# Performance work log

Measured on AMD Instinct MI355X. Metric: run time of the kernel, lower is better.

## Reference

```python
import jax, jax.numpy as jnp
import numpy as np

B, N = 64, 4096          # batch of diagrams, points per diagram
H, W = 64, 64            # persistence-image resolution
L, R = 5, 256            # num_landscapes, landscape resolution
EPS = 1e-8


def setup_inputs() -> dict:
    key = jax.random.key(0)
    k1, = jax.random.split(key, 1)
    u = jax.random.uniform(k1, (B, N, 2), dtype=jnp.float32)
    birth = u[..., 0] * 0.5                      # births in [0, 0.5]
    death = birth + u[..., 1] * 0.5 + 1e-3       # deaths > births, in range
    pairs = jnp.stack([birth, death], axis=-1)   # (B, N, 2)
    sigma = jnp.float32(0.1)                     # learned bandwidth (nn.Parameter)
    return {"pairs": pairs, "sigma": sigma}


def reference(pairs, sigma):
    # ---- Persistence image (batched, vectorized over points) ----
    grid_x = jnp.linspace(0.0, 1.0, W, dtype=pairs.dtype)   # birth axis
    grid_y = jnp.linspace(0.0, 1.0, H, dtype=pairs.dtype)   # persistence axis
    birth = pairs[..., 0]                 # (B, N)
    death = pairs[..., 1]                 # (B, N)
    pers = death - birth                  # (B, N)
    # normalization per config ranges (0,1): divide by (range + 1e-8)
    birth_n = birth / (1.0 + EPS)
    pers_n = pers / (1.0 + EPS)
    weights = pers                        # weight_fn == 'linear'
    inv2s2 = 1.0 / (2.0 * sigma * sigma)
    # separable Gaussian factors: (B, N, W) and (B, N, H)
    gx = jnp.exp(-(grid_x[None, None, :] - birth_n[..., None]) ** 2 * inv2s2)
    gy = jnp.exp(-(grid_y[None, None, :] - pers_n[..., None]) ** 2 * inv2s2)
    # sum_n wt_n * gy_n(h) * gx_n(w)  ->  (B, H, W)
    image = jnp.einsum('bnh,bnw->bhw', gy * weights[..., None], gx)
    image = image / (jnp.max(image, axis=(1, 2), keepdims=True) + EPS)

    # ---- Persistence landscapes ----
    min_b = jnp.min(birth, axis=1, keepdims=True)   # (B, 1)
    max_d = jnp.max(death, axis=1, keepdims=True)   # (B, 1)
    frac = jnp.linspace(0.0, 1.0, R, dtype=pairs.dtype)
    t = min_b + (max_d - min_b) * frac[None, :]     # (B, R)
    rising = jnp.clip(t[:, None, :] - birth[..., None], 0.0)   # (B, N, R)
    falling = jnp.clip(death[..., None] - t[:, None, :], 0.0)  # (B, N, R)
    tents = jnp.minimum(rising, falling)                        # (B, N, R)
    # descending sort over points + take top L == top_k over point axis
    top = jax.lax.top_k(jnp.swapaxes(tents, 1, 2), L)[0]        # (B, R, L)
    landscapes = jnp.swapaxes(top, 1, 2)                        # (B, L, R)
    return image, landscapes
```

## Files before the change

### kernel.cpp

```cpp
#include <hip/hip_runtime.h>
#include <math.h>


#define B_   64
#define N_   4096
#define HW_  64
#define RES_ 256
#define EPSF 1e-8f
#define KC_  4
#define CPB  1024
#define KP   64
#define LPB_ 8
#define LCH  128

typedef short short8v  __attribute__((ext_vector_type(8)));
typedef float float4v  __attribute__((ext_vector_type(4)));

__device__ __forceinline__ unsigned short f2bf(float f) {
    unsigned int u = __float_as_uint(f);
    u += 0x7fffu + ((u >> 16) & 1u);
    return (unsigned short)(u >> 16);
}

#define INS5(v0, v1, v2, v3, v4, x)                       \
    {                                                     \
        float _p0 = v0, _p1 = v1, _p2 = v2, _p3 = v3;     \
        v0 = fmaxf(_p0, x);                               \
        v1 = __builtin_amdgcn_fmed3f(_p0, _p1, x);        \
        v2 = __builtin_amdgcn_fmed3f(_p1, _p2, x);        \
        v3 = __builtin_amdgcn_fmed3f(_p2, _p3, x);        \
        v4 = __builtin_amdgcn_fmed3f(_p3, v4, x);         \
    }

union SmemU {
    struct {
        unsigned short gy[64 * 72];
        unsigned short gx[64 * 72];
        float2 pts[CPB];
    } img;
    struct {
        float lmerge[4 * 5 * RES_];
        float red[8];
    } land;
};

__global__ __launch_bounds__(256) void k_main(const float* __restrict__ pairs,
                                              const float* __restrict__ sigp,
                                              float* __restrict__ part,
                                              float* __restrict__ lp,
                                              int* __restrict__ ctr,
                                              float* __restrict__ out) {
    __shared__ SmemU sm;
    __shared__ int last_flag;
    __shared__ float redf[4];

    int tid = threadIdx.x;
    int l = tid & 63, w = tid >> 6;

    if (blockIdx.x < 256) {
        int kc = blockIdx.x & 3, b = blockIdx.x >> 2;
        float sigma = sigp[0];
        float cc = 0.5f / (sigma * sigma);

        const float4* src = (const float4*)(pairs + 2 * ((size_t)b * N_ + kc * CPB));
        ((float4*)sm.img.pts)[tid]       = src[tid];
        ((float4*)sm.img.pts)[256 + tid] = src[256 + tid];

        int c  = tid & 63;
        int pg = tid >> 6;
        float xc = (float)c * (1.0f / 63.0f);

        float4v acc[4];
        #pragma unroll
        for (int c4 = 0; c4 < 4; ++c4) acc[c4] = (float4v){0.f, 0.f, 0.f, 0.f};

        int rowA = (w * 16 + (l & 15)) * 72 + (l >> 4) * 8;

        for (int ch = 0; ch < CPB / KP; ++ch) {
            __syncthreads();
            int p0 = ch * KP + pg * 16;
            alignas(16) unsigned short gyb[16], gxb[16];
            #pragma unroll
            for (int j = 0; j < 16; ++j) {
                float2 q = sm.img.pts[p0 + j];
                float pe = q.y - q.x;
                float dx = xc - q.x;
                float dy = xc - pe;
                gxb[j] = f2bf(__expf(-dx * dx * cc));
                gyb[j] = f2bf(pe * __expf(-dy * dy * cc));
            }
            *(uint4*)&sm.img.gy[c * 72 + pg * 16]     = *(uint4*)&gyb[0];
            *(uint4*)&sm.img.gy[c * 72 + pg * 16 + 8] = *(uint4*)&gyb[8];
            *(uint4*)&sm.img.gx[c * 72 + pg * 16]     = *(uint4*)&gxb[0];
            *(uint4*)&sm.img.gx[c * 72 + pg * 16 + 8] = *(uint4*)&gxb[8];
            __syncthreads();
            #pragma unroll
            for (int ks = 0; ks < 2; ++ks) {
                short8v af = *(const short8v*)&sm.img.gy[rowA + ks * 32];
                #pragma unroll
                for (int c4 = 0; c4 < 4; ++c4) {
                    short8v bf = *(const short8v*)
                        &sm.img.gx[(c4 * 16 + (l & 15)) * 72 + ks * 32 + (l >> 4) * 8];
                    acc[c4] = __builtin_amdgcn_mfma_f32_16x16x32_bf16(af, bf, acc[c4], 0, 0, 0);
                }
            }
        }

        float* dst = part + (size_t)(b * KC_ + kc) * (HW_ * HW_);
        #pragma unroll
        for (int c4 = 0; c4 < 4; ++c4)
            #pragma unroll
            for (int reg = 0; reg < 4; ++reg) {
                int h = w * 16 + (l >> 4) * 4 + reg;
                int wv = c4 * 16 + (l & 15);
                dst[h * HW_ + wv] = acc[c4][reg];
            }

        __syncthreads();
        if (tid == 0) {
            int old = __hip_atomic_fetch_add(&ctr[b], 1, __ATOMIC_ACQ_REL,
                                             __HIP_MEMORY_SCOPE_AGENT);
            last_flag = (old == KC_ - 1);
        }
        __syncthreads();
        if (last_flag) {
            const float4* p0 = (const float4*)(part + (size_t)b * KC_ * (HW_ * HW_));
            float4 s[4];
            float m = 0.0f;
            #pragma unroll
            for (int i = 0; i < 4; ++i) {
                int pix4 = tid + i * 256;
                float4 v = p0[pix4];
                #pragma unroll
                for (int k2 = 1; k2 < KC_; ++k2) {
                    float4 u = p0[(size_t)k2 * 1024 + pix4];
                    v.x += u.x; v.y += u.y; v.z += u.z; v.w += u.w;
                }
                s[i] = v;
                m = fmaxf(m, fmaxf(fmaxf(v.x, v.y), fmaxf(v.z, v.w)));
            }
            #pragma unroll
            for (int off = 32; off > 0; off >>= 1) m = fmaxf(m, __shfl_xor(m, off, 64));
            if ((tid & 63) == 0) redf[tid >> 6] = m;
            __syncthreads();
            m = fmaxf(fmaxf(redf[0], redf[1]), fmaxf(redf[2], redf[3]));
            float inv = 1.0f / (m + EPSF);
            float4* od = (float4*)(out + (size_t)b * (HW_ * HW_));
            #pragma unroll
            for (int i = 0; i < 4; ++i) {
                float4 v = s[i];
                v.x *= inv; v.y *= inv; v.z *= inv; v.w *= inv;
                od[tid + i * 256] = v;
            }
        }
    } else {
        int idx = blockIdx.x - 256;
        int b = idx >> 3, pcb = idx & 7;

        const float4* pb4 = (const float4*)(pairs + 2 * (size_t)b * N_);
        float mn = 1e30f, mx = -1e30f;
        #pragma unroll
        for (int i = 0; i < 8; ++i) {
            float4 q = pb4[tid + i * 256];
            mn = fminf(mn, fminf(q.x, q.z));
            mx = fmaxf(mx, fmaxf(q.y, q.w));
        }
        #pragma unroll
        for (int off = 32; off > 0; off >>= 1) {
            mn = fminf(mn, __shfl_xor(mn, off, 64));
            mx = fmaxf(mx, __shfl_xor(mx, off, 64));
        }
        if ((tid & 63) == 0) { sm.land.red[w] = mn; sm.land.red[4 + w] = mx; }
        __syncthreads();
        float minb = fminf(fminf(sm.land.red[0], sm.land.red[1]),
                           fminf(sm.land.red[2], sm.land.red[3]));
        float maxd = fmaxf(fmaxf(sm.land.red[4], sm.land.red[5]),
                           fmaxf(sm.land.red[6], sm.land.red[7]));

        int pc = pcb * 4 + w;
        float scl = (maxd - minb) * (1.0f / 255.0f);
        float t0 = minb + scl * (float)l;
        float t1 = t0 + scl * 64.0f;
        float t2 = t0 + scl * 128.0f;
        float t3 = t0 + scl * 192.0f;

        float a0 = 0.f, a1 = 0.f, a2 = 0.f, a3 = 0.f, a4 = 0.f;
        float b0 = 0.f, b1 = 0.f, b2 = 0.f, b3 = 0.f, b4 = 0.f;
        float c0 = 0.f, c1 = 0.f, c2 = 0.f, c3 = 0.f, c4 = 0.f;
        float d0 = 0.f, d1 = 0.f, d2 = 0.f, d3 = 0.f, d4 = 0.f;

        const float4* pw = (const float4*)(pairs + 2 * ((size_t)b * N_ + pc * LCH));
        #pragma unroll 4
        for (int p = 0; p < LCH / 2; ++p) {
            float4 q = pw[p];
            {
                float bb = q.x, dd = q.y;
                float x;
                x = fminf(t0 - bb, dd - t0); INS5(a0, a1, a2, a3, a4, x);
                x = fminf(t1 - bb, dd - t1); INS5(b0, b1, b2, b3, b4, x);
                x = fminf(t2 - bb, dd - t2); INS5(c0, c1, c2, c3, c4, x);
                x = fminf(t3 - bb, dd - t3); INS5(d0, d1, d2, d3, d4, x);
            }
            {
                float bb = q.z, dd = q.w;
                float x;
                x = fminf(t0 - bb, dd - t0); INS5(a0, a1, a2, a3, a4, x);
                x = fminf(t1 - bb, dd - t1); INS5(b0, b1, b2, b3, b4, x);
                x = fminf(t2 - bb, dd - t2); INS5(c0, c1, c2, c3, c4, x);
                x = fminf(t3 - bb, dd - t3); INS5(d0, d1, d2, d3, d4, x);
            }
        }

        __syncthreads();
        float* lm = sm.land.lmerge;
        lm[(w * 5 + 0) * RES_ + l]       = a0; lm[(w * 5 + 1) * RES_ + l]       = a1;
        lm[(w * 5 + 2) * RES_ + l]       = a2; lm[(w * 5 + 3) * RES_ + l]       = a3;
        lm[(w * 5 + 4) * RES_ + l]       = a4;
        lm[(w * 5 + 0) * RES_ + l + 64]  = b0; lm[(w * 5 + 1) * RES_ + l + 64]  = b1;
        lm[(w * 5 + 2) * RES_ + l + 64]  = b2; lm[(w * 5 + 3) * RES_ + l + 64]  = b3;
        lm[(w * 5 + 4) * RES_ + l + 64]  = b4;
        lm[(w * 5 + 0) * RES_ + l + 128] = c0; lm[(w * 5 + 1) * RES_ + l + 128] = c1;
        lm[(w * 5 + 2) * RES_ + l + 128] = c2; lm[(w * 5 + 3) * RES_ + l + 128] = c3;
        lm[(w * 5 + 4) * RES_ + l + 128] = c4;
        lm[(w * 5 + 0) * RES_ + l + 192] = d0; lm[(w * 5 + 1) * RES_ + l + 192] = d1;
        lm[(w * 5 + 2) * RES_ + l + 192] = d2; lm[(w * 5 + 3) * RES_ + l + 192] = d3;
        lm[(w * 5 + 4) * RES_ + l + 192] = d4;
        __syncthreads();

        float v0 = lm[0 * RES_ + tid], v1 = lm[1 * RES_ + tid], v2 = lm[2 * RES_ + tid],
              v3 = lm[3 * RES_ + tid], v4 = lm[4 * RES_ + tid];
        #pragma unroll
        for (int wv = 1; wv < 4; ++wv)
            #pragma unroll
            for (int lvl = 0; lvl < 5; ++lvl) {
                float x = lm[(wv * 5 + lvl) * RES_ + tid];
                INS5(v0, v1, v2, v3, v4, x);
            }
        float* dl = lp + (size_t)(b * LPB_ + pcb) * 5 * RES_;
        dl[0 * RES_ + tid] = v0; dl[1 * RES_ + tid] = v1; dl[2 * RES_ + tid] = v2;
        dl[3 * RES_ + tid] = v3; dl[4 * RES_ + tid] = v4;

        __syncthreads();
        if (tid == 0) {
            int old = __hip_atomic_fetch_add(&ctr[64 + b], 1, __ATOMIC_ACQ_REL,
                                             __HIP_MEMORY_SCOPE_AGENT);
            last_flag = (old == LPB_ - 1);
        }
        __syncthreads();
        if (last_flag) {
            const float* lpb = lp + (size_t)b * LPB_ * 5 * RES_;
            float u0 = lpb[0 * RES_ + tid], u1 = lpb[1 * RES_ + tid],
                  u2 = lpb[2 * RES_ + tid], u3 = lpb[3 * RES_ + tid],
                  u4 = lpb[4 * RES_ + tid];
            for (int p2 = 1; p2 < LPB_; ++p2) {
                #pragma unroll
                for (int lvl = 0; lvl < 5; ++lvl) {
                    float x = lpb[(p2 * 5 + lvl) * RES_ + tid];
                    INS5(u0, u1, u2, u3, u4, x);
                }
            }
            float* o = out + (size_t)B_ * HW_ * HW_ + (size_t)b * (5 * RES_);
            o[tid]            = u0;
            o[RES_ + tid]     = u1;
            o[2 * RES_ + tid] = u2;
            o[3 * RES_ + tid] = u3;
            o[4 * RES_ + tid] = u4;
        }
    }
}

extern "C" void kernel_launch(void* const* d_in, const int* in_sizes, int n_in,
                              void* d_out, int out_size, void* d_ws, size_t ws_size,
                              hipStream_t stream) {
    const float* pairs = (const float*)d_in[0];
    const float* sig   = (const float*)d_in[1];
    float* out = (float*)d_out;
    float* wsf = (float*)d_ws;

    int*   ctr  = (int*)wsf;
    float* part = wsf + 128;
    float* lp   = part + (size_t)B_ * KC_ * HW_ * HW_;

    hipMemsetAsync(ctr, 0, 128 * sizeof(int), stream);
    k_main<<<768, 256, 0, stream>>>(pairs, sig, part, lp, ctr, out);
}
```

Baseline: 102.5 us.

## Split into partial and finish kernels, double block splits, interleave roles

```diff
diff --git a/kernel.cpp b/kernel.cpp
--- a/kernel.cpp
+++ b/kernel.cpp
@@ -7,19 +7,18 @@
 #define HW_  64
 #define RES_ 256
 #define EPSF 1e-8f
-#define KC_  4
-#define CPB  1024
+#define KC_  8
+#define CPB  512
 #define KP   64
-#define LPB_ 8
-#define LCH  128
+#define LPB_ 16
+#define LCH  64
 
 typedef short short8v  __attribute__((ext_vector_type(8)));
 typedef float float4v  __attribute__((ext_vector_type(4)));
 
-__device__ __forceinline__ unsigned short f2bf(float f) {
-    unsigned int u = __float_as_uint(f);
-    u += 0x7fffu + ((u >> 16) & 1u);
-    return (unsigned short)(u >> 16);
+__device__ __forceinline__ unsigned pk_bf(float a, float b) {
+    unsigned ua = __float_as_uint(a), ub = __float_as_uint(b);
+    return ((ua + 0x8000u) >> 16) | ((ub + 0x8000u) & 0xffff0000u);
 }
 
 #define INS5(v0, v1, v2, v3, v4, x)                       \
@@ -36,7 +35,6 @@
     struct {
         unsigned short gy[64 * 72];
         unsigned short gx[64 * 72];
-        float2 pts[CPB];
     } img;
     struct {
         float lmerge[4 * 5 * RES_];
@@ -44,27 +42,20 @@
     } land;
 };
 
-__global__ __launch_bounds__(256) void k_main(const float* __restrict__ pairs,
-                                              const float* __restrict__ sigp,
-                                              float* __restrict__ part,
-                                              float* __restrict__ lp,
-                                              int* __restrict__ ctr,
-                                              float* __restrict__ out) {
+__global__ __launch_bounds__(256) void k_partial(const float* __restrict__ pairs,
+                                                 const float* __restrict__ sigp,
+                                                 float* __restrict__ part,
+                                                 float* __restrict__ lp) {
     __shared__ SmemU sm;
-    __shared__ int last_flag;
-    __shared__ float redf[4];
-
     int tid = threadIdx.x;
     int l = tid & 63, w = tid >> 6;
-
-    if (blockIdx.x < 256) {
-        int kc = blockIdx.x & 3, b = blockIdx.x >> 2;
+    int role = blockIdx.x % 3;
+    int id   = blockIdx.x / 3;
+
+    if (role == 0) {
+        int kc = id & 7, b = id >> 3;
         float sigma = sigp[0];
-        float cc = 0.5f / (sigma * sigma);
-
-        const float4* src = (const float4*)(pairs + 2 * ((size_t)b * N_ + kc * CPB));
-        ((float4*)sm.img.pts)[tid]       = src[tid];
-        ((float4*)sm.img.pts)[256 + tid] = src[256 + tid];
+        float ncc2 = -(0.5f / (sigma * sigma)) * 1.4426950408889634f;
 
         int c  = tid & 63;
         int pg = tid >> 6;
@@ -75,24 +66,29 @@
         for (int c4 = 0; c4 < 4; ++c4) acc[c4] = (float4v){0.f, 0.f, 0.f, 0.f};
 
         int rowA = (w * 16 + (l & 15)) * 72 + (l >> 4) * 8;
+        const float4* pb4 = (const float4*)(pairs + 2 * ((size_t)b * N_ + kc * CPB));
 
         for (int ch = 0; ch < CPB / KP; ++ch) {
+            int p0 = ch * 32 + pg * 8;
+            unsigned gxp[8], gyp[8];
+            #pragma unroll
+            for (int jp = 0; jp < 8; ++jp) {
+                float4 q = pb4[p0 + jp];
+                float pe0 = q.y - q.x, pe1 = q.w - q.z;
+                float dx0 = xc - q.x, dx1 = xc - q.z;
+                float dy0 = xc - pe0, dy1 = xc - pe1;
+                float ex0 = __builtin_amdgcn_exp2f(dx0 * dx0 * ncc2);
+                float ex1 = __builtin_amdgcn_exp2f(dx1 * dx1 * ncc2);
+                float ey0 = pe0 * __builtin_amdgcn_exp2f(dy0 * dy0 * ncc2);
+                float ey1 = pe1 * __builtin_amdgcn_exp2f(dy1 * dy1 * ncc2);
+                gxp[jp] = pk_bf(ex0, ex1);
+                gyp[jp] = pk_bf(ey0, ey1);
+            }
             __syncthreads();
-            int p0 = ch * KP + pg * 16;
-            alignas(16) unsigned short gyb[16], gxb[16];
-            #pragma unroll
-            for (int j = 0; j < 16; ++j) {
-                float2 q = sm.img.pts[p0 + j];
-                float pe = q.y - q.x;
-                float dx = xc - q.x;
-                float dy = xc - pe;
-                gxb[j] = f2bf(__expf(-dx * dx * cc));
-                gyb[j] = f2bf(pe * __expf(-dy * dy * cc));
-            }
-            *(uint4*)&sm.img.gy[c * 72 + pg * 16]     = *(uint4*)&gyb[0];
-            *(uint4*)&sm.img.gy[c * 72 + pg * 16 + 8] = *(uint4*)&gyb[8];
-            *(uint4*)&sm.img.gx[c * 72 + pg * 16]     = *(uint4*)&gxb[0];
-            *(uint4*)&sm.img.gx[c * 72 + pg * 16 + 8] = *(uint4*)&gxb[8];
+            *(uint4*)&sm.img.gy[c * 72 + pg * 16]     = *(uint4*)&gyp[0];
+            *(uint4*)&sm.img.gy[c * 72 + pg * 16 + 8] = *(uint4*)&gyp[4];
+            *(uint4*)&sm.img.gx[c * 72 + pg * 16]     = *(uint4*)&gxp[0];
+            *(uint4*)&sm.img.gx[c * 72 + pg * 16 + 8] = *(uint4*)&gxp[4];
             __syncthreads();
             #pragma unroll
             for (int ks = 0; ks < 2; ++ks) {
@@ -115,47 +111,9 @@
                 int wv = c4 * 16 + (l & 15);
                 dst[h * HW_ + wv] = acc[c4][reg];
             }
-
-        __syncthreads();
-        if (tid == 0) {
-            int old = __hip_atomic_fetch_add(&ctr[b], 1, __ATOMIC_ACQ_REL,
-                                             __HIP_MEMORY_SCOPE_AGENT);
-            last_flag = (old == KC_ - 1);
-        }
-        __syncthreads();
-        if (last_flag) {
-            const float4* p0 = (const float4*)(part + (size_t)b * KC_ * (HW_ * HW_));
-            float4 s[4];
-            float m = 0.0f;
-            #pragma unroll
-            for (int i = 0; i < 4; ++i) {
-                int pix4 = tid + i * 256;
-                float4 v = p0[pix4];
-                #pragma unroll
-                for (int k2 = 1; k2 < KC_; ++k2) {
-                    float4 u = p0[(size_t)k2 * 1024 + pix4];
-                    v.x += u.x; v.y += u.y; v.z += u.z; v.w += u.w;
-                }
-                s[i] = v;
-                m = fmaxf(m, fmaxf(fmaxf(v.x, v.y), fmaxf(v.z, v.w)));
-            }
-            #pragma unroll
-            for (int off = 32; off > 0; off >>= 1) m = fmaxf(m, __shfl_xor(m, off, 64));
-            if ((tid & 63) == 0) redf[tid >> 6] = m;
-            __syncthreads();
-            m = fmaxf(fmaxf(redf[0], redf[1]), fmaxf(redf[2], redf[3]));
-            float inv = 1.0f / (m + EPSF);
-            float4* od = (float4*)(out + (size_t)b * (HW_ * HW_));
-            #pragma unroll
-            for (int i = 0; i < 4; ++i) {
-                float4 v = s[i];
-                v.x *= inv; v.y *= inv; v.z *= inv; v.w *= inv;
-                od[tid + i * 256] = v;
-            }
-        }
     } else {
-        int idx = blockIdx.x - 256;
-        int b = idx >> 3, pcb = idx & 7;
+        int idx = id * 2 + (role - 1);
+        int b = idx >> 4, pcb = idx & 15;
 
         const float4* pb4 = (const float4*)(pairs + 2 * (size_t)b * N_);
         float mn = 1e30f, mx = -1e30f;
@@ -211,7 +169,6 @@
             }
         }
 
-        __syncthreads();
         float* lm = sm.land.lmerge;
         lm[(w * 5 + 0) * RES_ + l]       = a0; lm[(w * 5 + 1) * RES_ + l]       = a1;
         lm[(w * 5 + 2) * RES_ + l]       = a2; lm[(w * 5 + 3) * RES_ + l]       = a3;
@@ -239,33 +196,63 @@
         float* dl = lp + (size_t)(b * LPB_ + pcb) * 5 * RES_;
         dl[0 * RES_ + tid] = v0; dl[1 * RES_ + tid] = v1; dl[2 * RES_ + tid] = v2;
         dl[3 * RES_ + tid] = v3; dl[4 * RES_ + tid] = v4;
-
+    }
+}
+
+__global__ __launch_bounds__(256) void k_finish(const float* __restrict__ part,
+                                                const float* __restrict__ lp,
+                                                float* __restrict__ out) {
+    __shared__ float redf[4];
+    int tid = threadIdx.x;
+    if (blockIdx.x < 64) {
+        int b = blockIdx.x;
+        const float4* p0 = (const float4*)(part + (size_t)b * KC_ * (HW_ * HW_));
+        float4 s[4];
+        float m = 0.0f;
+        #pragma unroll
+        for (int i = 0; i < 4; ++i) {
+            int pix4 = tid + i * 256;
+            float4 v = p0[pix4];
+            #pragma unroll
+            for (int k2 = 1; k2 < KC_; ++k2) {
+                float4 u = p0[(size_t)k2 * 1024 + pix4];
+                v.x += u.x; v.y += u.y; v.z += u.z; v.w += u.w;
+            }
+            s[i] = v;
+            m = fmaxf(m, fmaxf(fmaxf(v.x, v.y), fmaxf(v.z, v.w)));
+        }
+        #pragma unroll
+        for (int off = 32; off > 0; off >>= 1) m = fmaxf(m, __shfl_xor(m, off, 64));
+        if ((tid & 63) == 0) redf[tid >> 6] = m;
         __syncthreads();
-        if (tid == 0) {
-            int old = __hip_atomic_fetch_add(&ctr[64 + b], 1, __ATOMIC_ACQ_REL,
-                                             __HIP_MEMORY_SCOPE_AGENT);
-            last_flag = (old == LPB_ - 1);
-        }
-        __syncthreads();
-        if (last_flag) {
-            const float* lpb = lp + (size_t)b * LPB_ * 5 * RES_;
-            float u0 = lpb[0 * RES_ + tid], u1 = lpb[1 * RES_ + tid],
-                  u2 = lpb[2 * RES_ + tid], u3 = lpb[3 * RES_ + tid],
-                  u4 = lpb[4 * RES_ + tid];
-            for (int p2 = 1; p2 < LPB_; ++p2) {
-                #pragma unroll
-                for (int lvl = 0; lvl < 5; ++lvl) {
-                    float x = lpb[(p2 * 5 + lvl) * RES_ + tid];
-                    INS5(u0, u1, u2, u3, u4, x);
-                }
-            }
-            float* o = out + (size_t)B_ * HW_ * HW_ + (size_t)b * (5 * RES_);
-            o[tid]            = u0;
-            o[RES_ + tid]     = u1;
-            o[2 * RES_ + tid] = u2;
-            o[3 * RES_ + tid] = u3;
-            o[4 * RES_ + tid] = u4;
-        }
+        m = fmaxf(fmaxf(redf[0], redf[1]), fmaxf(redf[2], redf[3]));
+        float inv = 1.0f / (m + EPSF);
+        float4* od = (float4*)(out + (size_t)b * (HW_ * HW_));
+        #pragma unroll
+        for (int i = 0; i < 4; ++i) {
+            float4 v = s[i];
+            v.x *= inv; v.y *= inv; v.z *= inv; v.w *= inv;
+            od[tid + i * 256] = v;
+        }
+    } else {
+        int b = blockIdx.x - 64;
+        const float* lpb = lp + (size_t)b * LPB_ * 5 * RES_;
+        float u0 = lpb[0 * RES_ + tid], u1 = lpb[1 * RES_ + tid],
+              u2 = lpb[2 * RES_ + tid], u3 = lpb[3 * RES_ + tid],
+              u4 = lpb[4 * RES_ + tid];
+        for (int p2 = 1; p2 < LPB_; ++p2) {
+            #pragma unroll
+            for (int lvl = 0; lvl < 5; ++lvl) {
+                float x = lpb[(p2 * 5 + lvl) * RES_ + tid];
+                INS5(u0, u1, u2, u3, u4, x);
+            }
+        }
+        float* o = out + (size_t)B_ * HW_ * HW_ + (size_t)b * (5 * RES_);
+        o[tid]            = u0;
+        o[RES_ + tid]     = u1;
+        o[2 * RES_ + tid] = u2;
+        o[3 * RES_ + tid] = u3;
+        o[4 * RES_ + tid] = u4;
     }
 }
 
@@ -277,10 +264,9 @@
     float* out = (float*)d_out;
     float* wsf = (float*)d_ws;
 
-    int*   ctr  = (int*)wsf;
-    float* part = wsf + 128;
+    float* part = wsf;
     float* lp   = part + (size_t)B_ * KC_ * HW_ * HW_;
 
-    hipMemsetAsync(ctr, 0, 128 * sizeof(int), stream);
-    k_main<<<768, 256, 0, stream>>>(pairs, sig, part, lp, ctr, out);
-}
+    k_partial<<<1536, 256, 0, stream>>>(pairs, sig, part, lp);
+    k_finish<<<128, 256, 0, stream>>>(part, lp, out);
+}
```

Result: faster. 98.33 us (-4.1%).
